# Performance work log

Hardware: AMD Instinct MI355X
Metric: run time of the kernel (lower is better)

Reference implementation:

```python
import jax, jax.numpy as jnp
import numpy as np
from functools import partial

B, T, I, H = 64, 1024, 256, 256


def _lstm_dir(x_tbi, w_ih, w_hh, b_ih, b_hh, reverse):
    """Coupled-gate LSTM over time. x_tbi: [T,B,I]. Returns hs [T,B,H], (hT, cT).

    Gates = x@W_ih^T + b_ih + h@W_hh^T + b_hh, split into (in, cell, out);
    forget = 1 - in (coupled input/forget gates).
    """
    Bn = x_tbi.shape[1]
    Hn = w_hh.shape[1]
    # Precompute input contribution for all timesteps in one big GEMM.
    gx = jnp.einsum('tbi,gi->tbg', x_tbi, w_ih) + (b_ih + b_hh)  # [T,B,3H]

    def step(carry, g):
        h, c = carry
        gates = g + h @ w_hh.T  # [B,3H]
        ig, cg, og = jnp.split(gates, 3, axis=1)
        ig = jax.nn.sigmoid(ig)
        fg = 1.0 - ig
        cg = jnp.tanh(cg)
        og = jax.nn.sigmoid(og)
        c = fg * c + ig * cg
        h = og * jnp.tanh(c)
        return (h, c), h

    h0 = jnp.zeros((Bn, Hn), dtype=x_tbi.dtype)
    c0 = jnp.zeros((Bn, Hn), dtype=x_tbi.dtype)
    # lax.scan(reverse=True) runs backward in time but stacks outputs in
    # original time order, matching ReverseLSTMLayer's reverse(outputs).
    (hT, cT), hs = jax.lax.scan(step, (h0, c0), gx, reverse=reverse)
    return hs, hT, cT


def setup_inputs() -> dict:
    key = jax.random.key(0)
    ks = jax.random.split(key, 9)
    s = 0.05  # small init scale for numerical sanity
    return {
        'X': jax.random.normal(ks[0], (B, T, I), dtype=jnp.float32),
        'wih_f': jax.random.normal(ks[1], (3 * H, I), dtype=jnp.float32) * s,
        'whh_f': jax.random.normal(ks[2], (3 * H, H), dtype=jnp.float32) * s,
        'bih_f': jax.random.normal(ks[3], (3 * H,), dtype=jnp.float32) * s,
        'bhh_f': jax.random.normal(ks[4], (3 * H,), dtype=jnp.float32) * s,
        'wih_b': jax.random.normal(ks[5], (3 * H, I), dtype=jnp.float32) * s,
        'whh_b': jax.random.normal(ks[6], (3 * H, H), dtype=jnp.float32) * s,
        'bih_b': jax.random.normal(ks[7], (3 * H,), dtype=jnp.float32) * s,
        'bhh_b': jax.random.normal(ks[8], (3 * H,), dtype=jnp.float32) * s,
    }


def reference(X, wih_f, whh_f, bih_f, bhh_f, wih_b, whh_b, bih_b, bhh_b):
    x_tbi = jnp.transpose(X, (1, 0, 2))  # [T,B,I]
    hs_f, hTf, cTf = _lstm_dir(x_tbi, wih_f, whh_f, bih_f, bhh_f, reverse=False)
    hs_b, hTb, cTb = _lstm_dir(x_tbi, wih_b, whh_b, bih_b, bhh_b, reverse=True)
    out = jnp.concatenate([hs_f, hs_b], axis=-1)  # [T,B,2H]
    hn = jnp.concatenate([hTf, hTb], axis=1)[None]  # [1,B,2H]
    cn = jnp.concatenate([cTf, cTb], axis=1)[None]
    return out, hn, cn
```

## Files before the change

kernel.cpp:

```cpp
#include <hip/hip_runtime.h>
#include <cstdint>
#include <cstddef>

#define TT 1024
#define NB 64
#define HD 256
#define NG 768

typedef short bhalf8 __attribute__((ext_vector_type(8)));
typedef float f32x4  __attribute__((ext_vector_type(4)));

#define LOG2E  1.4426950408889634f
#define LOG2E2 2.8853900817779268f

__device__ __forceinline__ float bf2f(unsigned short s) {
  return __uint_as_float(((unsigned)s) << 16);
}
__device__ __forceinline__ unsigned cvt_pk_bf16(float lo, float hi) {
  unsigned r;
  asm("v_cvt_pk_bf16_f32 %0, %1, %2" : "=v"(r) : "v"(lo), "v"(hi));
  return r;
}
__device__ __forceinline__ float clamp24(float x) {
  return fminf(fmaxf(x, -24.0f), 24.0f);
}
__device__ __forceinline__ void inv4(float d0, float d1, float d2, float d3,
                                     float& i0, float& i1, float& i2, float& i3) {
  float p2 = d0 * d1;
  float p3 = p2 * d2;
  float p4 = p3 * d3;
  float r  = __builtin_amdgcn_rcpf(p4);
  i3 = r * p3;
  float r3 = r * d3;
  i2 = r3 * p2;
  float r2 = r3 * d2;
  i1 = r2 * d0;
  i0 = r2 * d1;
}

#define GX_SLICE ((size_t)TT * NG * 16)

__launch_bounds__(256, 2)
__global__ void gx_kernel(const float* __restrict__ X,
                          const float* __restrict__ wih_f, const float* __restrict__ bih_f,
                          const float* __restrict__ bhh_f,
                          const float* __restrict__ wih_b, const float* __restrict__ bih_b,
                          const float* __restrict__ bhh_b,
                          unsigned short* __restrict__ gx) {
  const int tid = threadIdx.x;
  const int n0  = blockIdx.x * 64;
  const int t0  = blockIdx.y * 4;

  __shared__ unsigned short Al[64][264];
  __shared__ unsigned short Bl[64][264];

  const int lane = tid & 63, w = tid >> 6, quad = lane >> 4, l15 = lane & 15;
  const float wsc = (n0 >= 256 && n0 < 512) ? LOG2E2 : LOG2E;

  for (int dir = 0; dir < 2; ++dir) {
    const float* wih = dir ? wih_b : wih_f;
    const float* bih = dir ? bih_b : bih_f;
    const float* bhh = dir ? bhh_b : bhh_f;
    unsigned short* gxd = gx + (size_t)dir * 4 * GX_SLICE;

    __syncthreads();
#pragma unroll
    for (int i = 0; i < 16; ++i) {
      int f4  = tid + i * 256;
      int row = f4 >> 6;
      int kk  = (f4 & 63) * 4;
      float4 wv = *(const float4*)(wih + (size_t)(n0 + row) * HD + kk);
      uint2 p;
      p.x = cvt_pk_bf16(wv.x * wsc, wv.y * wsc);
      p.y = cvt_pk_bf16(wv.z * wsc, wv.w * wsc);
      *(uint2*)&Bl[row][kk] = p;
    }

    for (int tt = 0; tt < 4; ++tt) {
      const int t = t0 + tt;
      __syncthreads();
#pragma unroll
      for (int i = 0; i < 16; ++i) {
        int f4  = tid + i * 256;
        int row = f4 >> 6;
        int kk  = (f4 & 63) * 4;
        float4 xv = *(const float4*)(X + ((size_t)row * TT + t) * HD + kk);
        uint2 p;
        p.x = cvt_pk_bf16(xv.x, xv.y);
        p.y = cvt_pk_bf16(xv.z, xv.w);
        *(uint2*)&Al[row][kk] = p;
      }
      __syncthreads();

      f32x4 acc[4];
#pragma unroll
      for (int jt = 0; jt < 4; ++jt) { acc[jt][0]=0.f; acc[jt][1]=0.f; acc[jt][2]=0.f; acc[jt][3]=0.f; }

#pragma unroll
      for (int kt = 0; kt < 8; ++kt) {
        bhalf8 a = *(const bhalf8*)&Al[16 * w + l15][kt * 32 + quad * 8];
#pragma unroll
        for (int jt = 0; jt < 4; ++jt) {
          bhalf8 b = *(const bhalf8*)&Bl[jt * 16 + l15][kt * 32 + quad * 8];
          acc[jt] = __builtin_amdgcn_mfma_f32_16x16x32_bf16(a, b, acc[jt], 0, 0, 0);
        }
      }

      unsigned short* gs = gxd + w * GX_SLICE + (size_t)t * NG * 16;
#pragma unroll
      for (int jt = 0; jt < 4; ++jt) {
        int g = n0 + jt * 16 + l15;
        float bias = (bih[g] + bhh[g]) * wsc;
        uint2 p;
        p.x = cvt_pk_bf16(acc[jt][0] + bias, acc[jt][1] + bias);
        p.y = cvt_pk_bf16(acc[jt][2] + bias, acc[jt][3] + bias);
        *(uint2*)(gs + g * 16 + quad * 4) = p;
      }
    }
  }
}

__attribute__((amdgpu_flat_work_group_size(512, 512)))
__attribute__((amdgpu_waves_per_eu(2, 2)))
__global__ void rec_kernel(const float* __restrict__ whh_f,
                           const float* __restrict__ whh_b,
                           const unsigned short* __restrict__ gx,
                           float* __restrict__ out) {
  const int tid  = threadIdx.x;
  const int lane = tid & 63, w = tid >> 6, quad = lane >> 4, l15 = lane & 15;
  const int blk = blockIdx.x;
  const int dir = blk >> 2;
  const int b0  = (blk & 3) * 16;
  const float* whh = dir ? whh_b : whh_f;
  const unsigned short* gxd = gx + (size_t)dir * 4 * GX_SLICE + (size_t)(blk & 3) * GX_SLICE;
  float* hn = out + (size_t)TT * NB * 512;
  float* cn = hn + (size_t)NB * 512;

  __shared__ uint4 wlds[8][8][64];
  __shared__ uint4 hk[2][8][64];

  bhalf8 wreg[5][8];
#pragma unroll
  for (int p = 0; p < 6; ++p) {
    int n = (p >> 1) * 256 + 32 * w + (p & 1) * 16 + l15;
    const float wscp = ((p >> 1) == 1) ? LOG2E2 : LOG2E;
#pragma unroll
    for (int kt = 0; kt < 8; ++kt) {
      const float* wp = whh + (size_t)n * HD + kt * 32 + quad * 8;
      float4 v0 = *(const float4*)wp;
      float4 v1 = *(const float4*)(wp + 4);
      union { bhalf8 v; uint4 u; } pk;
      pk.u.x = cvt_pk_bf16(v0.x * wscp, v0.y * wscp);
      pk.u.y = cvt_pk_bf16(v0.z * wscp, v0.w * wscp);
      pk.u.z = cvt_pk_bf16(v1.x * wscp, v1.y * wscp);
      pk.u.w = cvt_pk_bf16(v1.z * wscp, v1.w * wscp);
      if (p < 5) wreg[p][kt] = pk.v;
      else       wlds[w][kt][lane] = pk.u;
    }
  }

  {
    uint4 z; z.x = z.y = z.z = z.w = 0;
    for (int i = tid; i < 8 * 64; i += 512) ((uint4*)hk[0])[i] = z;
  }

  float cstate[2][4];
#pragma unroll
  for (int jn = 0; jn < 2; ++jn)
#pragma unroll
    for (int r = 0; r < 4; ++r) cstate[jn][r] = 0.0f;

  int goff[6];
#pragma unroll
  for (int p = 0; p < 6; ++p) {
    int g = (p >> 1) * 256 + 32 * w + (p & 1) * 16 + l15;
    goff[p] = g * 16 + quad * 4;
  }

  __syncthreads();

  const unsigned short* gptr = gxd + (size_t)(dir ? (TT - 1) : 0) * NG * 16;
  const ptrdiff_t gstep = dir ? -(ptrdiff_t)((size_t)NG * 16) : (ptrdiff_t)((size_t)NG * 16);

  float* orow = out + ((size_t)(dir ? (TT - 1) : 0) * NB + b0 + quad * 4) * 512
                + dir * 256 + 32 * w + l15;
  const ptrdiff_t ostep = dir ? -(ptrdiff_t)(NB * 512) : (ptrdiff_t)(NB * 512);

  ushort4 gxv[6];
#pragma unroll
  for (int p = 0; p < 6; ++p) gxv[p] = *(const ushort4*)(gptr + goff[p]);

#pragma unroll 2
  for (int s = 0; s < TT; ++s) {
    const int pb = s & 1;

    f32x4 acc[6];
#pragma unroll
    for (int p = 0; p < 6; ++p) {
      acc[p][0] = bf2f(gxv[p].x); acc[p][1] = bf2f(gxv[p].y);
      acc[p][2] = bf2f(gxv[p].z); acc[p][3] = bf2f(gxv[p].w);
    }
    gptr += gstep;
#pragma unroll
    for (int p = 0; p < 6; ++p) gxv[p] = *(const ushort4*)(gptr + goff[p]);

#pragma unroll
    for (int kt = 0; kt < 8; ++kt) {
      bhalf8 a = __builtin_bit_cast(bhalf8, hk[pb][kt][lane]);
#pragma unroll
      for (int p = 0; p < 5; ++p)
        acc[p] = __builtin_amdgcn_mfma_f32_16x16x32_bf16(a, wreg[p][kt], acc[p], 0, 0, 0);
      acc[5] = __builtin_amdgcn_mfma_f32_16x16x32_bf16(
          a, __builtin_bit_cast(bhalf8, wlds[w][kt][lane]), acc[5], 0, 0, 0);
    }

    unsigned short* hnext = (unsigned short*)hk[pb ^ 1][w];
#pragma unroll
    for (int jn = 0; jn < 2; ++jn) {
      float ei[4], ec[4], eo[4];
#pragma unroll
      for (int r = 0; r < 4; ++r) {
        ei[r] = __builtin_amdgcn_exp2f(clamp24(-acc[jn][r]));
        ec[r] = __builtin_amdgcn_exp2f(clamp24( acc[2 + jn][r]));
        eo[r] = __builtin_amdgcn_exp2f(clamp24(-acc[4 + jn][r]));
      }
      float ig[4], tc[4], og[4];
      inv4(1.f + ei[0], 1.f + ei[1], 1.f + ei[2], 1.f + ei[3],
           ig[0], ig[1], ig[2], ig[3]);
      inv4(1.f + ec[0], 1.f + ec[1], 1.f + ec[2], 1.f + ec[3],
           tc[0], tc[1], tc[2], tc[3]);
      inv4(1.f + eo[0], 1.f + eo[1], 1.f + eo[2], 1.f + eo[3],
           og[0], og[1], og[2], og[3]);
      float cvv[4], et[4];
#pragma unroll
      for (int r = 0; r < 4; ++r) {
        float cg = __builtin_fmaf(-2.f, tc[r], 1.f);
        float cp = cstate[jn][r];
        float cv = __builtin_fmaf(ig[r], cg - cp, cp);
        cstate[jn][r] = cv;
        cvv[r] = cv;
        et[r] = __builtin_amdgcn_exp2f(cv * LOG2E2);
      }
      float it4[4];
      inv4(1.f + et[0], 1.f + et[1], 1.f + et[2], 1.f + et[3],
           it4[0], it4[1], it4[2], it4[3]);
      float hv[4];
#pragma unroll
      for (int r = 0; r < 4; ++r)
        hv[r] = og[r] * __builtin_fmaf(-2.f, it4[r], 1.f);

      unsigned short* hbj = hnext + (size_t)(((jn * 2 + (l15 >> 3)) * 16 + quad * 4) * 8)
                            + (l15 & 7);
      unsigned u01 = cvt_pk_bf16(hv[0], hv[1]);
      unsigned u23 = cvt_pk_bf16(hv[2], hv[3]);
      hbj[0]  = (unsigned short)u01;
      hbj[8]  = (unsigned short)(u01 >> 16);
      hbj[16] = (unsigned short)u23;
      hbj[24] = (unsigned short)(u23 >> 16);

#pragma unroll
      for (int r = 0; r < 4; ++r) {
        orow[(size_t)r * 512 + jn * 16] = hv[r];
        if (s == TT - 1) {
          int brow = b0 + quad * 4 + r;
          int col  = 32 * w + jn * 16 + l15;
          hn[(size_t)brow * 512 + dir * 256 + col] = hv[r];
          cn[(size_t)brow * 512 + dir * 256 + col] = cvv[r];
        }
      }
    }
    orow += ostep;
    __syncthreads();
  }
}

extern "C" void kernel_launch(void* const* d_in, const int* in_sizes, int n_in,
                              void* d_out, int out_size, void* d_ws, size_t ws_size,
                              hipStream_t stream) {
  const float* X     = (const float*)d_in[0];
  const float* wih_f = (const float*)d_in[1];
  const float* whh_f = (const float*)d_in[2];
  const float* bih_f = (const float*)d_in[3];
  const float* bhh_f = (const float*)d_in[4];
  const float* wih_b = (const float*)d_in[5];
  const float* whh_b = (const float*)d_in[6];
  const float* bih_b = (const float*)d_in[7];
  const float* bhh_b = (const float*)d_in[8];
  float* out = (float*)d_out;
  unsigned short* gxbuf = (unsigned short*)d_ws;

  dim3 g1(NG / 64, TT / 4);
  gx_kernel<<<g1, 256, 0, stream>>>(X, wih_f, bih_f, bhh_f, wih_b, bih_b, bhh_b, gxbuf);
  rec_kernel<<<8, 512, 0, stream>>>(whh_f, whh_b, gxbuf, out);
}
```

Before: 2.314 ms.

## Split recurrent kernel across 16 waves per block, one gate tile each

The recurrent kernel now runs 1024 threads per block (16 waves), each wave owning 16 hidden columns instead of 32. Per-wave MFMA work and activation math per timestep are halved, which shortens the serial critical path of each step. The cost is a 16-wave barrier each step and fewer registers per thread, since waves_per_eu rises to 4. The clamp is also switched to a single med3 instruction.

```diff
diff --git a/kernel.cpp b/kernel.cpp
--- a/kernel.cpp
+++ b/kernel.cpp
@@ -22,7 +22,7 @@
   return r;
 }
 __device__ __forceinline__ float clamp24(float x) {
-  return fminf(fmaxf(x, -24.0f), 24.0f);
+  return __builtin_amdgcn_fmed3f(x, -24.0f, 24.0f);
 }
 __device__ __forceinline__ void inv4(float d0, float d1, float d2, float d3,
                                      float& i0, float& i1, float& i2, float& i3) {
@@ -120,8 +120,8 @@
   }
 }
 
-__attribute__((amdgpu_flat_work_group_size(512, 512)))
-__attribute__((amdgpu_waves_per_eu(2, 2)))
+__attribute__((amdgpu_flat_work_group_size(1024, 1024)))
+__attribute__((amdgpu_waves_per_eu(4, 4)))
 __global__ void rec_kernel(const float* __restrict__ whh_f,
                            const float* __restrict__ whh_b,
                            const unsigned short* __restrict__ gx,
@@ -136,14 +136,14 @@
   float* hn = out + (size_t)TT * NB * 512;
   float* cn = hn + (size_t)NB * 512;
 
-  __shared__ uint4 wlds[8][8][64];
+  __shared__ uint4 wlds[16][8][64];
   __shared__ uint4 hk[2][8][64];
 
-  bhalf8 wreg[5][8];
-#pragma unroll
-  for (int p = 0; p < 6; ++p) {
-    int n = (p >> 1) * 256 + 32 * w + (p & 1) * 16 + l15;
-    const float wscp = ((p >> 1) == 1) ? LOG2E2 : LOG2E;
+  bhalf8 wreg[2][8];
+#pragma unroll
+  for (int p = 0; p < 3; ++p) {
+    int n = p * 256 + 16 * w + l15;
+    const float wscp = (p == 1) ? LOG2E2 : LOG2E;
 #pragma unroll
     for (int kt = 0; kt < 8; ++kt) {
       const float* wp = whh + (size_t)n * HD + kt * 32 + quad * 8;
@@ -154,26 +154,24 @@
       pk.u.y = cvt_pk_bf16(v0.z * wscp, v0.w * wscp);
       pk.u.z = cvt_pk_bf16(v1.x * wscp, v1.y * wscp);
       pk.u.w = cvt_pk_bf16(v1.z * wscp, v1.w * wscp);
-      if (p < 5) wreg[p][kt] = pk.v;
+      if (p < 2) wreg[p][kt] = pk.v;
       else       wlds[w][kt][lane] = pk.u;
     }
   }
 
-  {
+  if (tid < 512) {
     uint4 z; z.x = z.y = z.z = z.w = 0;
-    for (int i = tid; i < 8 * 64; i += 512) ((uint4*)hk[0])[i] = z;
-  }
-
-  float cstate[2][4];
-#pragma unroll
-  for (int jn = 0; jn < 2; ++jn)
-#pragma unroll
-    for (int r = 0; r < 4; ++r) cstate[jn][r] = 0.0f;
-
-  int goff[6];
-#pragma unroll
-  for (int p = 0; p < 6; ++p) {
-    int g = (p >> 1) * 256 + 32 * w + (p & 1) * 16 + l15;
+    ((uint4*)hk[0])[tid] = z;
+  }
+
+  float cstate[4];
+#pragma unroll
+  for (int r = 0; r < 4; ++r) cstate[r] = 0.0f;
+
+  int goff[3];
+#pragma unroll
+  for (int p = 0; p < 3; ++p) {
+    int g = p * 256 + 16 * w + l15;
     goff[p] = g * 16 + quad * 4;
   }
 
@@ -183,90 +181,86 @@
   const ptrdiff_t gstep = dir ? -(ptrdiff_t)((size_t)NG * 16) : (ptrdiff_t)((size_t)NG * 16);
 
   float* orow = out + ((size_t)(dir ? (TT - 1) : 0) * NB + b0 + quad * 4) * 512
-                + dir * 256 + 32 * w + l15;
+                + dir * 256 + 16 * w + l15;
   const ptrdiff_t ostep = dir ? -(ptrdiff_t)(NB * 512) : (ptrdiff_t)(NB * 512);
 
-  ushort4 gxv[6];
-#pragma unroll
-  for (int p = 0; p < 6; ++p) gxv[p] = *(const ushort4*)(gptr + goff[p]);
+  ushort4 gxv[3];
+#pragma unroll
+  for (int p = 0; p < 3; ++p) gxv[p] = *(const ushort4*)(gptr + goff[p]);
 
 #pragma unroll 2
   for (int s = 0; s < TT; ++s) {
     const int pb = s & 1;
 
-    f32x4 acc[6];
-#pragma unroll
-    for (int p = 0; p < 6; ++p) {
+    f32x4 acc[3];
+#pragma unroll
+    for (int p = 0; p < 3; ++p) {
       acc[p][0] = bf2f(gxv[p].x); acc[p][1] = bf2f(gxv[p].y);
       acc[p][2] = bf2f(gxv[p].z); acc[p][3] = bf2f(gxv[p].w);
     }
     gptr += gstep;
 #pragma unroll
-    for (int p = 0; p < 6; ++p) gxv[p] = *(const ushort4*)(gptr + goff[p]);
+    for (int p = 0; p < 3; ++p) gxv[p] = *(const ushort4*)(gptr + goff[p]);
 
 #pragma unroll
     for (int kt = 0; kt < 8; ++kt) {
       bhalf8 a = __builtin_bit_cast(bhalf8, hk[pb][kt][lane]);
-#pragma unroll
-      for (int p = 0; p < 5; ++p)
-        acc[p] = __builtin_amdgcn_mfma_f32_16x16x32_bf16(a, wreg[p][kt], acc[p], 0, 0, 0);
-      acc[5] = __builtin_amdgcn_mfma_f32_16x16x32_bf16(
-          a, __builtin_bit_cast(bhalf8, wlds[w][kt][lane]), acc[5], 0, 0, 0);
-    }
-
-    unsigned short* hnext = (unsigned short*)hk[pb ^ 1][w];
-#pragma unroll
-    for (int jn = 0; jn < 2; ++jn) {
-      float ei[4], ec[4], eo[4];
-#pragma unroll
-      for (int r = 0; r < 4; ++r) {
-        ei[r] = __builtin_amdgcn_exp2f(clamp24(-acc[jn][r]));
-        ec[r] = __builtin_amdgcn_exp2f(clamp24( acc[2 + jn][r]));
-        eo[r] = __builtin_amdgcn_exp2f(clamp24(-acc[4 + jn][r]));
-      }
-      float ig[4], tc[4], og[4];
-      inv4(1.f + ei[0], 1.f + ei[1], 1.f + ei[2], 1.f + ei[3],
-           ig[0], ig[1], ig[2], ig[3]);
-      inv4(1.f + ec[0], 1.f + ec[1], 1.f + ec[2], 1.f + ec[3],
-           tc[0], tc[1], tc[2], tc[3]);
-      inv4(1.f + eo[0], 1.f + eo[1], 1.f + eo[2], 1.f + eo[3],
-           og[0], og[1], og[2], og[3]);
-      float cvv[4], et[4];
-#pragma unroll
-      for (int r = 0; r < 4; ++r) {
-        float cg = __builtin_fmaf(-2.f, tc[r], 1.f);
-        float cp = cstate[jn][r];
-        float cv = __builtin_fmaf(ig[r], cg - cp, cp);
-        cstate[jn][r] = cv;
-        cvv[r] = cv;
-        et[r] = __builtin_amdgcn_exp2f(cv * LOG2E2);
-      }
-      float it4[4];
-      inv4(1.f + et[0], 1.f + et[1], 1.f + et[2], 1.f + et[3],
-           it4[0], it4[1], it4[2], it4[3]);
-      float hv[4];
-#pragma unroll
-      for (int r = 0; r < 4; ++r)
-        hv[r] = og[r] * __builtin_fmaf(-2.f, it4[r], 1.f);
-
-      unsigned short* hbj = hnext + (size_t)(((jn * 2 + (l15 >> 3)) * 16 + quad * 4) * 8)
-                            + (l15 & 7);
-      unsigned u01 = cvt_pk_bf16(hv[0], hv[1]);
-      unsigned u23 = cvt_pk_bf16(hv[2], hv[3]);
-      hbj[0]  = (unsigned short)u01;
-      hbj[8]  = (unsigned short)(u01 >> 16);
-      hbj[16] = (unsigned short)u23;
-      hbj[24] = (unsigned short)(u23 >> 16);
-
-#pragma unroll
-      for (int r = 0; r < 4; ++r) {
-        orow[(size_t)r * 512 + jn * 16] = hv[r];
-        if (s == TT - 1) {
-          int brow = b0 + quad * 4 + r;
-          int col  = 32 * w + jn * 16 + l15;
-          hn[(size_t)brow * 512 + dir * 256 + col] = hv[r];
-          cn[(size_t)brow * 512 + dir * 256 + col] = cvv[r];
-        }
+      acc[0] = __builtin_amdgcn_mfma_f32_16x16x32_bf16(a, wreg[0][kt], acc[0], 0, 0, 0);
+      acc[1] = __builtin_amdgcn_mfma_f32_16x16x32_bf16(a, wreg[1][kt], acc[1], 0, 0, 0);
+      acc[2] = __builtin_amdgcn_mfma_f32_16x16x32_bf16(
+          a, __builtin_bit_cast(bhalf8, wlds[w][kt][lane]), acc[2], 0, 0, 0);
+    }
+
+    unsigned short* hnext = (unsigned short*)hk[pb ^ 1][w >> 1];
+    float ei[4], ec[4], eo[4];
+#pragma unroll
+    for (int r = 0; r < 4; ++r) {
+      ei[r] = __builtin_amdgcn_exp2f(clamp24(-acc[0][r]));
+      ec[r] = __builtin_amdgcn_exp2f(clamp24( acc[1][r]));
+      eo[r] = __builtin_amdgcn_exp2f(clamp24(-acc[2][r]));
+    }
+    float ig[4], tc[4], og[4];
+    inv4(1.f + ei[0], 1.f + ei[1], 1.f + ei[2], 1.f + ei[3],
+         ig[0], ig[1], ig[2], ig[3]);
+    inv4(1.f + ec[0], 1.f + ec[1], 1.f + ec[2], 1.f + ec[3],
+         tc[0], tc[1], tc[2], tc[3]);
+    inv4(1.f + eo[0], 1.f + eo[1], 1.f + eo[2], 1.f + eo[3],
+         og[0], og[1], og[2], og[3]);
+    float cvv[4], et[4];
+#pragma unroll
+    for (int r = 0; r < 4; ++r) {
+      float cg = __builtin_fmaf(-2.f, tc[r], 1.f);
+      float cp = cstate[r];
+      float cv = __builtin_fmaf(ig[r], cg - cp, cp);
+      cstate[r] = cv;
+      cvv[r] = cv;
+      et[r] = __builtin_amdgcn_exp2f(cv * LOG2E2);
+    }
+    float it4[4];
+    inv4(1.f + et[0], 1.f + et[1], 1.f + et[2], 1.f + et[3],
+         it4[0], it4[1], it4[2], it4[3]);
+    float hv[4];
+#pragma unroll
+    for (int r = 0; r < 4; ++r)
+      hv[r] = og[r] * __builtin_fmaf(-2.f, it4[r], 1.f);
+
+    unsigned short* hbj = hnext
+        + (size_t)(((((w & 1) * 2 + (l15 >> 3)) * 16) + quad * 4) * 8) + (l15 & 7);
+    unsigned u01 = cvt_pk_bf16(hv[0], hv[1]);
+    unsigned u23 = cvt_pk_bf16(hv[2], hv[3]);
+    hbj[0]  = (unsigned short)u01;
+    hbj[8]  = (unsigned short)(u01 >> 16);
+    hbj[16] = (unsigned short)u23;
+    hbj[24] = (unsigned short)(u23 >> 16);
+
+#pragma unroll
+    for (int r = 0; r < 4; ++r) {
+      orow[(size_t)r * 512 + 0] = hv[r];
+      if (s == TT - 1) {
+        int brow = b0 + quad * 4 + r;
+        int col  = 16 * w + l15;
+        hn[(size_t)brow * 512 + dir * 256 + col] = hv[r];
+        cn[(size_t)brow * 512 + dir * 256 + col] = cvv[r];
       }
     }
     orow += ostep;
@@ -291,5 +285,5 @@
 
   dim3 g1(NG / 64, TT / 4);
   gx_kernel<<<g1, 256, 0, stream>>>(X, wih_f, bih_f, bhh_f, wih_b, bih_b, bhh_b, gxbuf);
-  rec_kernel<<<8, 512, 0, stream>>>(whh_f, whh_b, gxbuf, out);
-}
+  rec_kernel<<<8, 1024, 0, stream>>>(whh_f, whh_b, gxbuf, out);
+}
```

Measured after the change: 1.920 ms. 1.21x faster.
